# Kernel tuning notes

Measured on AMD Instinct MI355X. Metric: run time of the kernel, lower is better.

Reference implementation:

```python
import jax, jax.numpy as jnp
import numpy as np

DMODEL = 1024
NHEADS = 16
FFN = 4 * DMODEL
HEAD_DIM = DMODEL // NHEADS
SCALE = HEAD_DIM ** -0.5


def layer_norm(x, gamma, beta, eps=1e-5):
    mu = jnp.mean(x, axis=-1, keepdims=True)
    var = jnp.var(x, axis=-1, keepdims=True)
    return (x - mu) * jax.lax.rsqrt(var + eps) * gamma + beta


def setup_inputs() -> dict:
    key = jax.random.key(0)
    ks = jax.random.split(key, 8)
    std = 0.02
    B, S = 2, 2048
    return {
        "src": jax.random.normal(ks[0], (B, S, DMODEL), jnp.float32),
        "pre_gamma": jnp.ones((DMODEL,), jnp.float32),
        "pre_beta": jnp.zeros((DMODEL,), jnp.float32),
        "qkv_w": jax.random.truncated_normal(ks[1], -2.0, 2.0, (3 * DMODEL, DMODEL), jnp.float32) * std,
        "qkv_b": jnp.zeros((3 * DMODEL,), jnp.float32),
        "addnorm_gamma": jnp.ones((DMODEL,), jnp.float32),
        "addnorm_beta": jnp.zeros((DMODEL,), jnp.float32),
        "fc1_w": jax.random.truncated_normal(ks[2], -2.0, 2.0, (FFN, DMODEL), jnp.float32) * std,
        "fc1_b": jnp.zeros((FFN,), jnp.float32),
        "fc2_w": jax.random.truncated_normal(ks[3], -2.0, 2.0, (DMODEL, FFN), jnp.float32) * std,
        "fc2_b": jnp.zeros((DMODEL,), jnp.float32),
    }


def reference(src, pre_gamma, pre_beta, qkv_w, qkv_b, addnorm_gamma, addnorm_beta,
              fc1_w, fc1_b, fc2_w, fc2_b):
    B, S, D = src.shape
    # PreNorm
    x = layer_norm(src, pre_gamma, pre_beta)
    # MHSA (no output projection, matching source)
    qkv = x @ qkv_w.T + qkv_b  # [B,S,3D]
    q, k, v = jnp.split(qkv, 3, axis=-1)
    def heads(t):
        return t.reshape(B, S, NHEADS, HEAD_DIM).transpose(0, 2, 1, 3)  # [B,H,S,hd]
    q, k, v = heads(q), heads(k), heads(v)
    attn = jnp.einsum("bhqd,bhkd->bhqk", q, k) * SCALE
    attn = jax.nn.softmax(attn, axis=-1)
    attn_out = jnp.einsum("bhqk,bhkd->bhqd", attn, v)
    attn_out = attn_out.transpose(0, 2, 1, 3).reshape(B, S, D)
    # shared AddNorm #1
    x = layer_norm(attn_out + x, addnorm_gamma, addnorm_beta)
    # FFN
    h = jax.nn.gelu(x @ fc1_w.T + fc1_b, approximate=False)
    ffn_out = h @ fc2_w.T + fc2_b
    # shared AddNorm #2 (same params as #1)
    return layer_norm(ffn_out + x, addnorm_gamma, addnorm_beta)
```

## Files before the change

### kernel.cpp

```cpp
#include <hip/hip_runtime.h>
#include <hip/hip_bf16.h>
#include <math.h>

#define DMODEL 1024
#define NH 16
#define HD 64
#define SEQ 2048
#define BATCH 2
#define MROWS (BATCH * SEQ)
#define FFN_DIM 4096

using bf16x8 = __attribute__((ext_vector_type(8))) __bf16;
using f32x4  = __attribute__((ext_vector_type(4))) float;

typedef const __attribute__((address_space(1))) unsigned char* gas_t;
typedef __attribute__((address_space(3))) unsigned char* las_t;

__device__ inline unsigned short f2bf(float f) {
    unsigned int u = __builtin_bit_cast(unsigned int, f);
    u += 0x7fffu + ((u >> 16) & 1u);
    return (unsigned short)(u >> 16);
}
__device__ inline unsigned short f2bf_up(float f) {
    unsigned int u = __builtin_bit_cast(unsigned int, f);
    return (unsigned short)((u + 0x8000u) >> 16);
}
__device__ inline float bf2f(unsigned short u) {
    unsigned int v = ((unsigned int)u) << 16;
    return __builtin_bit_cast(float, v);
}
__device__ inline float gelu_f(float x) {
    float x2 = x * x;
    float w = x * fmaf(0.07135481627f, x2, 1.59576912161f);
    return x / (1.0f + __expf(-w));
}

__global__ __launch_bounds__(256) void ln_pre_cvt(
        const float* __restrict__ a,
        const float* __restrict__ gamma, const float* __restrict__ beta,
        float* __restrict__ out_f, unsigned short* __restrict__ out_b,
        const float* __restrict__ wa, unsigned short* __restrict__ oa, int na4,
        const float* __restrict__ wb, unsigned short* __restrict__ ob, int nb4,
        const float* __restrict__ wc, unsigned char* __restrict__ oc, int nc4) {
    int blk = blockIdx.x;
    int t = threadIdx.x;
    if (blk >= MROWS) {
        int i = (blk - MROWS) * 256 + t;
        if (i < na4) {
            float4 v = ((const float4*)wa)[i];
            ushort4 o;
            o.x = f2bf(v.x); o.y = f2bf(v.y); o.z = f2bf(v.z); o.w = f2bf(v.w);
            ((ushort4*)oa)[i] = o;
        } else if (i < na4 + nb4) {
            int j = i - na4;
            float4 v = ((const float4*)wb)[j];
            ushort4 o;
            o.x = f2bf(v.x); o.y = f2bf(v.y); o.z = f2bf(v.z); o.w = f2bf(v.w);
            ((ushort4*)ob)[j] = o;
        } else if (i < na4 + nb4 + nc4) {
            int j = i - na4 - nb4;
            float4 v = ((const float4*)wc)[j];
            int pk = __builtin_amdgcn_cvt_pk_fp8_f32(v.x, v.y, 0, false);
            pk     = __builtin_amdgcn_cvt_pk_fp8_f32(v.z, v.w, pk, true);
            ((unsigned int*)oc)[j] = (unsigned int)pk;
        }
        return;
    }
    int row = blk;
    float4 v = ((const float4*)(a + (size_t)row * DMODEL))[t];
    float s  = v.x + v.y + v.z + v.w;
    float s2 = v.x * v.x + v.y * v.y + v.z * v.z + v.w * v.w;
    #pragma unroll
    for (int off = 32; off > 0; off >>= 1) {
        s  += __shfl_xor(s,  off, 64);
        s2 += __shfl_xor(s2, off, 64);
    }
    __shared__ float red[8];
    int wave = t >> 6, lane = t & 63;
    if (lane == 0) { red[wave] = s; red[4 + wave] = s2; }
    __syncthreads();
    float tot  = red[0] + red[1] + red[2] + red[3];
    float tot2 = red[4] + red[5] + red[6] + red[7];
    float mu   = tot * (1.0f / DMODEL);
    float var  = tot2 * (1.0f / DMODEL) - mu * mu;
    float rstd = rsqrtf(var + 1e-5f);
    float4 g  = ((const float4*)gamma)[t];
    float4 be = ((const float4*)beta)[t];
    float4 o;
    o.x = (v.x - mu) * rstd * g.x + be.x;
    o.y = (v.y - mu) * rstd * g.y + be.y;
    o.z = (v.z - mu) * rstd * g.z + be.z;
    o.w = (v.w - mu) * rstd * g.w + be.w;
    ((float4*)(out_f + (size_t)row * DMODEL))[t] = o;
    ushort4 ob4;
    ob4.x = f2bf(o.x); ob4.y = f2bf(o.y); ob4.z = f2bf(o.z); ob4.w = f2bf(o.w);
    ((ushort4*)(out_b + (size_t)row * DMODEL))[t] = ob4;
}

__global__ __launch_bounds__(256) void ln_attn(
        const float* __restrict__ o0, const float* __restrict__ o1,
        const float* __restrict__ l0, const float* __restrict__ l1,
        const float* __restrict__ xres,
        const float* __restrict__ gamma, const float* __restrict__ beta,
        float* __restrict__ out_f, unsigned short* __restrict__ out_b) {
    int row = blockIdx.x;
    int t = threadIdx.x;
    int b_ = row >> 11, s = row & 2047;
    int h = t >> 4;
    int bh = b_ * NH + h;
    size_t obase = ((size_t)bh * SEQ + s) * HD + (4 * t & 63);
    float4 va = ((const float4*)(o0 + obase))[0];
    float4 vb = ((const float4*)(o1 + obase))[0];
    float inv_l = 1.0f / (l0[(size_t)bh * SEQ + s] + l1[(size_t)bh * SEQ + s]);
    float4 rr = ((const float4*)(xres + (size_t)row * DMODEL))[t];
    float4 v;
    v.x = (va.x + vb.x) * inv_l + rr.x;
    v.y = (va.y + vb.y) * inv_l + rr.y;
    v.z = (va.z + vb.z) * inv_l + rr.z;
    v.w = (va.w + vb.w) * inv_l + rr.w;

    float s1 = v.x + v.y + v.z + v.w;
    float s2 = v.x * v.x + v.y * v.y + v.z * v.z + v.w * v.w;
    #pragma unroll
    for (int off = 32; off > 0; off >>= 1) {
        s1 += __shfl_xor(s1, off, 64);
        s2 += __shfl_xor(s2, off, 64);
    }
    __shared__ float red[8];
    int wave = t >> 6, lane = t & 63;
    if (lane == 0) { red[wave] = s1; red[4 + wave] = s2; }
    __syncthreads();
    float tot  = red[0] + red[1] + red[2] + red[3];
    float tot2 = red[4] + red[5] + red[6] + red[7];
    float mu   = tot * (1.0f / DMODEL);
    float var  = tot2 * (1.0f / DMODEL) - mu * mu;
    float rstd = rsqrtf(var + 1e-5f);
    float4 g  = ((const float4*)gamma)[t];
    float4 be = ((const float4*)beta)[t];
    float4 o;
    o.x = (v.x - mu) * rstd * g.x + be.x;
    o.y = (v.y - mu) * rstd * g.y + be.y;
    o.z = (v.z - mu) * rstd * g.z + be.z;
    o.w = (v.w - mu) * rstd * g.w + be.w;
    ((float4*)(out_f + (size_t)row * DMODEL))[t] = o;
    ushort4 ob;
    ob.x = f2bf(o.x); ob.y = f2bf(o.y); ob.z = f2bf(o.z); ob.w = f2bf(o.w);
    ((ushort4*)(out_b + (size_t)row * DMODEL))[t] = ob;
}

__global__ __launch_bounds__(256) void ln_fc2(
        const unsigned short* __restrict__ p0, const unsigned short* __restrict__ p1,
        const unsigned short* __restrict__ p2, const unsigned short* __restrict__ p3,
        const float* __restrict__ bias, const float* __restrict__ resid,
        const float* __restrict__ gamma, const float* __restrict__ beta,
        float* __restrict__ out_f) {
    int row = blockIdx.x;
    int t = threadIdx.x;
    size_t base = (size_t)row * DMODEL;
    ushort4 u0 = ((const ushort4*)(p0 + base))[t];
    ushort4 u1 = ((const ushort4*)(p1 + base))[t];
    ushort4 u2 = ((const ushort4*)(p2 + base))[t];
    ushort4 u3 = ((const ushort4*)(p3 + base))[t];
    float4 bb = ((const float4*)bias)[t];
    float4 rr = ((const float4*)(resid + base))[t];
    float4 v;
    v.x = bf2f(u0.x) + bf2f(u1.x) + bf2f(u2.x) + bf2f(u3.x) + bb.x + rr.x;
    v.y = bf2f(u0.y) + bf2f(u1.y) + bf2f(u2.y) + bf2f(u3.y) + bb.y + rr.y;
    v.z = bf2f(u0.z) + bf2f(u1.z) + bf2f(u2.z) + bf2f(u3.z) + bb.z + rr.z;
    v.w = bf2f(u0.w) + bf2f(u1.w) + bf2f(u2.w) + bf2f(u3.w) + bb.w + rr.w;

    float s  = v.x + v.y + v.z + v.w;
    float s2 = v.x * v.x + v.y * v.y + v.z * v.z + v.w * v.w;
    #pragma unroll
    for (int off = 32; off > 0; off >>= 1) {
        s  += __shfl_xor(s,  off, 64);
        s2 += __shfl_xor(s2, off, 64);
    }
    __shared__ float red[8];
    int wave = t >> 6, lane = t & 63;
    if (lane == 0) { red[wave] = s; red[4 + wave] = s2; }
    __syncthreads();
    float tot  = red[0] + red[1] + red[2] + red[3];
    float tot2 = red[4] + red[5] + red[6] + red[7];
    float mu   = tot * (1.0f / DMODEL);
    float var  = tot2 * (1.0f / DMODEL) - mu * mu;
    float rstd = rsqrtf(var + 1e-5f);
    float4 g  = ((const float4*)gamma)[t];
    float4 be = ((const float4*)beta)[t];
    float4 o;
    o.x = (v.x - mu) * rstd * g.x + be.x;
    o.y = (v.y - mu) * rstd * g.y + be.y;
    o.z = (v.z - mu) * rstd * g.z + be.z;
    o.w = (v.w - mu) * rstd * g.w + be.w;
    ((float4*)(out_f + base))[t] = o;
}

template <int MODE>
__global__ __launch_bounds__(256) void gemm_lds(
        const unsigned short* __restrict__ A,
        const unsigned short* __restrict__ Bw,
        const float* __restrict__ bias,
        void* __restrict__ out, int M, int N, int K) {
    __shared__ unsigned short As[2][128 * 64];
    __shared__ unsigned short Bs[2][128 * 64];

    const int tid  = threadIdx.x;
    const int wave = tid >> 6;
    const int lane = tid & 63;
    const int quad = lane >> 4;
    const int cc   = lane & 15;
    const int bn = blockIdx.x * 128;
    const int bm = blockIdx.y * 128;

    const unsigned short* Ab = A  + (size_t)bm * K;
    const unsigned short* Bb = Bw + (size_t)bn * K;

    const int srow0 = tid >> 3;
    const int sslot = tid & 7;
    const int rsw   = (cc >> 1) & 7;
    const int wm = (wave >> 1) * 64;
    const int wn = (wave & 1) * 64;

    f32x4 acc[4][4] = {};

    auto stage = [&](int buf, int k0) {
        #pragma unroll
        for (int i = 0; i < 4; ++i) {
            int row = i * 32 + srow0;
            int g   = sslot ^ ((row >> 1) & 7);
            const unsigned short* ga = Ab + (size_t)row * K + k0 + g * 8;
            const unsigned short* gb = Bb + (size_t)row * K + k0 + g * 8;
            unsigned short* la = &As[buf][i * 2048 + wave * 512];
            unsigned short* lb = &Bs[buf][i * 2048 + wave * 512];
            __builtin_amdgcn_global_load_lds((gas_t)(const void*)ga, (las_t)(void*)la, 16, 0, 0);
            __builtin_amdgcn_global_load_lds((gas_t)(const void*)gb, (las_t)(void*)lb, 16, 0, 0);
        }
    };

    const int nkt = K >> 6;
    stage(0, 0);
    __syncthreads();

    int cur = 0;
    for (int kt = 0; kt < nkt; ++kt) {
        if (kt + 1 < nkt) stage(cur ^ 1, (kt + 1) << 6);

        bf16x8 af[4][2], bf[4][2];
        #pragma unroll
        for (int mt = 0; mt < 4; ++mt)
            #pragma unroll
            for (int s = 0; s < 2; ++s) {
                int slot = (s * 4 + quad) ^ rsw;
                af[mt][s] = *(const bf16x8*)&As[cur][(wm + mt * 16 + cc) * 64 + slot * 8];
            }
        #pragma unroll
        for (int nt = 0; nt < 4; ++nt)
            #pragma unroll
            for (int s = 0; s < 2; ++s) {
                int slot = (s * 4 + quad) ^ rsw;
                bf[nt][s] = *(const bf16x8*)&Bs[cur][(wn + nt * 16 + cc) * 64 + slot * 8];
            }

        #pragma unroll
        for (int mt = 0; mt < 4; ++mt)
            #pragma unroll
            for (int nt = 0; nt < 4; ++nt) {
                acc[mt][nt] = __builtin_amdgcn_mfma_f32_16x16x32_bf16(
                    af[mt][0], bf[nt][0], acc[mt][nt], 0, 0, 0);
                acc[mt][nt] = __builtin_amdgcn_mfma_f32_16x16x32_bf16(
                    af[mt][1], bf[nt][1], acc[mt][nt], 0, 0, 0);
            }

        if (kt + 1 < nkt) __syncthreads();
        cur ^= 1;
    }

    #pragma unroll
    for (int mt = 0; mt < 4; ++mt)
        #pragma unroll
        for (int nt = 0; nt < 4; ++nt) {
            if constexpr (MODE == 1) {
                int m0 = bm + wm + mt * 16 + quad * 4;
                int n  = bn + wn + nt * 16 + cc;
                float bn_ = bias[n];
                float v0 = gelu_f(acc[mt][nt][0] + bn_);
                float v1 = gelu_f(acc[mt][nt][1] + bn_);
                float v2 = gelu_f(acc[mt][nt][2] + bn_);
                float v3 = gelu_f(acc[mt][nt][3] + bn_);
                int pk = __builtin_amdgcn_cvt_pk_fp8_f32(v0, v1, 0, false);
                pk     = __builtin_amdgcn_cvt_pk_fp8_f32(v2, v3, pk, true);
                unsigned char* o = (unsigned char*)out + (size_t)m0 * N + n;
                o[0]             = (unsigned char)pk;
                o[(size_t)N]     = (unsigned char)(pk >> 8);
                o[(size_t)2 * N] = (unsigned char)(pk >> 16);
                o[(size_t)3 * N] = (unsigned char)(pk >> 24);
            } else {
                #pragma unroll
                for (int r = 0; r < 4; ++r) {
                    int m = bm + wm + mt * 16 + quad * 4 + r;
                    int n = bn + wn + nt * 16 + cc;
                    float v = acc[mt][nt][r] + bias[n];
                    int b_ = m >> 11, srow = m & 2047;
                    int which = n >> 10, rem = n & 1023;
                    int h = rem >> 6, d = rem & 63;
                    if (which == 0) v *= 0.125f;
                    size_t idx = ((((size_t)which * BATCH + b_) * NH + h) * SEQ + srow) * HD + d;
                    ((unsigned short*)out)[idx] = f2bf(v);
                }
            }
        }
}

__global__ __launch_bounds__(256) void gemm_fp8(
        const unsigned char* __restrict__ A,
        const unsigned char* __restrict__ Bw,
        unsigned short* __restrict__ p0, unsigned short* __restrict__ p1,
        unsigned short* __restrict__ p2, unsigned short* __restrict__ p3,
        int M, int N, int K, int KC) {
    __shared__ unsigned char As[3][128 * 64];
    __shared__ unsigned char Bs[3][128 * 64];

    const int tid  = threadIdx.x;
    const int wave = tid >> 6;
    const int lane = tid & 63;
    const int quad = lane >> 4;
    const int cc   = lane & 15;
    const int bn = blockIdx.x * 128;
    const int bm = blockIdx.y * 128;

    const unsigned char* Ab = A  + (size_t)bm * K;
    const unsigned char* Bb = Bw + (size_t)bn * K;

    const int srow0 = tid >> 2;
    const int schunk = tid & 3;
    const int rsw = (cc >> 1) & 3;
    const int wm = (wave >> 1) * 64;
    const int wn = (wave & 1) * 64;

    const int kbeg = blockIdx.z * KC;

    f32x4 acc[4][4] = {};

    auto stage = [&](int buf, int k0) {
        #pragma unroll
        for (int i = 0; i < 2; ++i) {
            int row = i * 64 + srow0;
            int g   = schunk ^ ((row >> 1) & 3);
            const unsigned char* ga = Ab + (size_t)row * K + k0 + g * 16;
            const unsigned char* gb = Bb + (size_t)row * K + k0 + g * 16;
            unsigned char* la = &As[buf][i * 4096 + wave * 1024];
            unsigned char* lb = &Bs[buf][i * 4096 + wave * 1024];
            __builtin_amdgcn_global_load_lds((gas_t)(const void*)ga, (las_t)(void*)la, 16, 0, 0);
            __builtin_amdgcn_global_load_lds((gas_t)(const void*)gb, (las_t)(void*)lb, 16, 0, 0);
        }
    };

    const int nkt = KC >> 6;
    stage(0, kbeg);
    if (nkt > 1) {
        stage(1, kbeg + 64);
        asm volatile("s_waitcnt vmcnt(4)" ::: "memory");
    } else {
        asm volatile("s_waitcnt vmcnt(0)" ::: "memory");
    }
    __builtin_amdgcn_s_barrier();

    int cur = 0;
    for (int kt = 0; kt < nkt; ++kt) {
        int pbuf = cur + 2; if (pbuf >= 3) pbuf -= 3;
        if (kt + 2 < nkt) stage(pbuf, kbeg + ((kt + 2) << 6));

        long af[4][2], bf[4][2];
        #pragma unroll
        for (int mt = 0; mt < 4; ++mt)
            #pragma unroll
            for (int s = 0; s < 2; ++s) {
                int slot = ((quad >> 1) + 2 * s) ^ rsw;
                af[mt][s] = *(const long*)&As[cur][(wm + mt * 16 + cc) * 64 + slot * 16 + (quad & 1) * 8];
            }
        #pragma unroll
        for (int nt = 0; nt < 4; ++nt)
            #pragma unroll
            for (int s = 0; s < 2; ++s) {
                int slot = ((quad >> 1) + 2 * s) ^ rsw;
                bf[nt][s] = *(const long*)&Bs[cur][(wn + nt * 16 + cc) * 64 + slot * 16 + (quad & 1) * 8];
            }

        #pragma unroll
        for (int mt = 0; mt < 4; ++mt)
            #pragma unroll
            for (int nt = 0; nt < 4; ++nt) {
                acc[mt][nt] = __builtin_amdgcn_mfma_f32_16x16x32_fp8_fp8(
                    af[mt][0], bf[nt][0], acc[mt][nt], 0, 0, 0);
                acc[mt][nt] = __builtin_amdgcn_mfma_f32_16x16x32_fp8_fp8(
                    af[mt][1], bf[nt][1], acc[mt][nt], 0, 0, 0);
            }

        if (kt + 1 < nkt) {
            asm volatile("s_waitcnt lgkmcnt(0)" ::: "memory");
            if (kt + 2 < nkt)
                asm volatile("s_waitcnt vmcnt(4)" ::: "memory");
            else
                asm volatile("s_waitcnt vmcnt(0)" ::: "memory");
            __builtin_amdgcn_s_barrier();
        }
        cur = (cur < 2) ? cur + 1 : 0;
    }

    unsigned short* outp = (blockIdx.z == 0) ? p0
                         : (blockIdx.z == 1) ? p1
                         : (blockIdx.z == 2) ? p2 : p3;
    #pragma unroll
    for (int mt = 0; mt < 4; ++mt)
        #pragma unroll
        for (int nt = 0; nt < 4; ++nt)
            #pragma unroll
            for (int r = 0; r < 4; ++r) {
                int m = bm + wm + mt * 16 + quad * 4 + r;
                int n = bn + wn + nt * 16 + cc;
                outp[(size_t)m * N + n] = f2bf(acc[mt][nt][r]);
            }
}

__global__ __launch_bounds__(256) void transpose_v(
        const unsigned short* __restrict__ vsrc, unsigned short* __restrict__ vt) {
    __shared__ unsigned short Ls[64 * 72];
    const int t = threadIdx.x;
    const int s0 = blockIdx.x * 64;
    const int bh = blockIdx.y;
    const unsigned short* in = vsrc + (size_t)bh * SEQ * HD;
    unsigned short* outp = vt + (size_t)bh * SEQ * HD;

    const int row = t >> 2;
    const int c8  = (t & 3) * 8;
    #pragma unroll
    for (int p = 0; p < 2; ++p)
        *(uint4*)&Ls[row * 72 + c8 + p * 32] =
            *(const uint4*)&in[(size_t)(s0 + row) * HD + c8 + p * 32];
    __syncthreads();

    const int hd = t >> 2;
    #pragma unroll
    for (int p = 0; p < 2; ++p) {
        unsigned short tmp[8];
        #pragma unroll
        for (int j = 0; j < 8; ++j)
            tmp[j] = Ls[(c8 + p * 32 + j) * 72 + hd];
        *(uint4*)&outp[(size_t)hd * SEQ + s0 + c8 + p * 32] = *(uint4*)tmp;
    }
}

#define KPAD 72
__global__ __launch_bounds__(256, 4) void attn_mfma(
        const unsigned short* __restrict__ qkv,
        const unsigned short* __restrict__ vt,
        float* __restrict__ op0, float* __restrict__ op1,
        float* __restrict__ lpart) {
    const int tid  = threadIdx.x;
    const int wave = tid >> 6;
    const int lane = tid & 63;
    const int quad = lane >> 4;
    const int cc   = lane & 15;
    const int qblk = blockIdx.x;
    const int bh   = blockIdx.y;
    const int half = blockIdx.z;

    const size_t headsz = (size_t)SEQ * HD;
    const unsigned short* qb  = qkv + (size_t)bh * headsz;
    const unsigned short* kb  = qkv + ((size_t)BATCH * NH + bh) * headsz;
    const unsigned short* vtb = vt + (size_t)bh * headsz;
    float* opart = half ? op1 : op0;
    float* lp    = lpart + (size_t)half * BATCH * NH * SEQ;

    __shared__ unsigned short Ks[64 * 64];
    __shared__ unsigned short Vt[64 * 64];
    __shared__ unsigned short Ps[4 * 32 * KPAD];

    bf16x8 qa[2][2];
    #pragma unroll
    for (int mt = 0; mt < 2; ++mt) {
        const unsigned short* qp =
            qb + (size_t)(qblk * 128 + wave * 32 + mt * 16 + cc) * HD + quad * 8;
        qa[mt][0] = *(const bf16x8*)qp;
        qa[mt][1] = *(const bf16x8*)(qp + 32);
    }

    f32x4 o_acc[2][4] = {};
    float l_i[2][4] = {};

    const int srow0 = wave * 16 + (lane >> 3);
    const int sc8c  = lane & 7;
    const int swz   = (sc8c ^ (lane >> 3)) * 8;
    const int psw   = (cc >> 2) & 3;
    const int rw7   = cc & 7;

    const int kt0 = half * 16, ktend = kt0 + 16;

    uint4 ka0, ka1, va0, va1;
    {
        const unsigned short* kp0 = &kb[(size_t)(kt0 * 64 + srow0) * HD + sc8c * 8];
        const unsigned short* vp0 = &vtb[(size_t)srow0 * SEQ + kt0 * 64 + sc8c * 8];
        ka0 = *(const uint4*)kp0;
        ka1 = *(const uint4*)(kp0 + 8 * HD);
        va0 = *(const uint4*)vp0;
        va1 = *(const uint4*)(vp0 + 8 * SEQ);
    }

    for (int kt = kt0; kt < ktend; ++kt) {
        __syncthreads();
        *(uint4*)&Ks[srow0 * 64 + swz]        = ka0;
        *(uint4*)&Ks[(srow0 + 8) * 64 + swz]  = ka1;
        *(uint4*)&Vt[srow0 * 64 + swz]        = va0;
        *(uint4*)&Vt[(srow0 + 8) * 64 + swz]  = va1;
        __syncthreads();

        int ktn = (kt + 1 < ktend) ? kt + 1 : kt;
        const unsigned short* kpn = &kb[(size_t)(ktn * 64 + srow0) * HD + sc8c * 8];
        const unsigned short* vpn = &vtb[(size_t)srow0 * SEQ + ktn * 64 + sc8c * 8];
        uint4 nk0 = *(const uint4*)kpn;
        uint4 nk1 = *(const uint4*)(kpn + 8 * HD);
        uint4 nv0 = *(const uint4*)vpn;
        uint4 nv1 = *(const uint4*)(vpn + 8 * SEQ);

        f32x4 s_acc[2][4];
        #pragma unroll
        for (int nt = 0; nt < 4; ++nt) {
            const unsigned short* kp = &Ks[(nt * 16 + cc) * 64];
            bf16x8 kf0 = *(const bf16x8*)&kp[(quad ^ rw7) * 8];
            bf16x8 kf1 = *(const bf16x8*)&kp[((quad + 4) ^ rw7) * 8];
            #pragma unroll
            for (int mt = 0; mt < 2; ++mt) {
                f32x4 z = {};
                z = __builtin_amdgcn_mfma_f32_16x16x32_bf16(qa[mt][0], kf0, z, 0, 0, 0);
                s_acc[mt][nt] = __builtin_amdgcn_mfma_f32_16x16x32_bf16(qa[mt][1], kf1, z, 0, 0, 0);
            }
        }

        unsigned short* pw = &Ps[wave * 32 * KPAD];
        #pragma unroll
        for (int mt = 0; mt < 2; ++mt)
            #pragma unroll
            for (int nt = 0; nt < 4; ++nt) {
                int pc = ((nt ^ quad) & 3) * 16 + cc;
                #pragma unroll
                for (int r = 0; r < 4; ++r) {
                    float e = __expf(s_acc[mt][nt][r]);
                    l_i[mt][r] += e;
                    pw[(mt * 16 + quad * 4 + r) * KPAD + pc] = f2bf_up(e);
                }
            }

        bf16x8 pf[2][2];
        #pragma unroll
        for (int mt = 0; mt < 2; ++mt) {
            const unsigned short* pa = &pw[(mt * 16 + cc) * KPAD];
            pf[mt][0] = *(const bf16x8*)&pa[((((quad >> 1))     ^ psw) & 3) * 16 + (quad & 1) * 8];
            pf[mt][1] = *(const bf16x8*)&pa[(((2 + (quad >> 1)) ^ psw) & 3) * 16 + (quad & 1) * 8];
        }

        #pragma unroll
        for (int nt = 0; nt < 4; ++nt) {
            const unsigned short* vp = &Vt[(nt * 16 + cc) * 64];
            bf16x8 vf0 = *(const bf16x8*)&vp[(quad ^ rw7) * 8];
            bf16x8 vf1 = *(const bf16x8*)&vp[((quad + 4) ^ rw7) * 8];
            #pragma unroll
            for (int mt = 0; mt < 2; ++mt) {
                o_acc[mt][nt] = __builtin_amdgcn_mfma_f32_16x16x32_bf16(
                    pf[mt][0], vf0, o_acc[mt][nt], 0, 0, 0);
                o_acc[mt][nt] = __builtin_amdgcn_mfma_f32_16x16x32_bf16(
                    pf[mt][1], vf1, o_acc[mt][nt], 0, 0, 0);
            }
        }

        ka0 = nk0; ka1 = nk1; va0 = nv0; va1 = nv1;
    }

    #pragma unroll
    for (int mt = 0; mt < 2; ++mt) {
        float lr[4];
        #pragma unroll
        for (int r = 0; r < 4; ++r) {
            float l = l_i[mt][r];
            #pragma unroll
            for (int off = 1; off < 16; off <<= 1)
                l += __shfl_xor(l, off, 64);
            lr[r] = l;
        }
        int rowbase = qblk * 128 + wave * 32 + mt * 16;
        if (cc == 0) {
            float4 lv = {lr[0], lr[1], lr[2], lr[3]};
            *(float4*)&lp[(size_t)bh * SEQ + rowbase + quad * 4] = lv;
        }
        #pragma unroll
        for (int nt = 0; nt < 4; ++nt)
            #pragma unroll
            for (int r = 0; r < 4; ++r) {
                int row = rowbase + quad * 4 + r;
                opart[((size_t)bh * SEQ + row) * HD + nt * 16 + cc] = o_acc[mt][nt][r];
            }
    }
}

extern "C" void kernel_launch(void* const* d_in, const int* in_sizes, int n_in,
                              void* d_out, int out_size, void* d_ws, size_t ws_size,
                              hipStream_t stream) {
    const float* src       = (const float*)d_in[0];
    const float* pre_gamma = (const float*)d_in[1];
    const float* pre_beta  = (const float*)d_in[2];
    const float* qkv_w     = (const float*)d_in[3];
    const float* qkv_b     = (const float*)d_in[4];
    const float* an_gamma  = (const float*)d_in[5];
    const float* an_beta   = (const float*)d_in[6];
    const float* fc1_w     = (const float*)d_in[7];
    const float* fc1_b     = (const float*)d_in[8];
    const float* fc2_w     = (const float*)d_in[9];
    const float* fc2_b     = (const float*)d_in[10];
    float* out = (float*)d_out;

    char* ws = (char*)d_ws;
    size_t off = 0;
    auto alloc = [&](size_t bytes) {
        char* p = ws + off;
        off += (bytes + 255) & ~(size_t)255;
        return p;
    };
    float*          x_f   = (float*)alloc((size_t)MROWS * DMODEL * 4);
    unsigned short* x_b   = (unsigned short*)alloc((size_t)MROWS * DMODEL * 2);
    float*          y_f   = (float*)alloc((size_t)MROWS * DMODEL * 4);
    unsigned short* y_b   = (unsigned short*)alloc((size_t)MROWS * DMODEL * 2);
    float*          atf   = (float*)alloc((size_t)MROWS * DMODEL * 4);
    float*          fff   = (float*)alloc((size_t)MROWS * DMODEL * 4);
    unsigned short* qkvb  = (unsigned short*)alloc((size_t)3 * MROWS * DMODEL * 2);
    unsigned char*  h8    = (unsigned char*)alloc((size_t)MROWS * FFN_DIM * 2);
    unsigned short* wqkv  = (unsigned short*)alloc((size_t)3 * DMODEL * DMODEL * 2);
    unsigned short* wfc1  = (unsigned short*)alloc((size_t)FFN_DIM * DMODEL * 2);
    unsigned char*  wfc28 = (unsigned char*)alloc((size_t)DMODEL * FFN_DIM);

    unsigned short* vt_b = (unsigned short*)fff;
    float* opart0 = atf;
    float* opart1 = (float*)h8;
    float* lpart  = (float*)x_b;
    unsigned short* fc2p0 = (unsigned short*)fff;
    unsigned short* fc2p1 = (unsigned short*)x_f;
    unsigned short* fc2p2 = (unsigned short*)atf;
    unsigned short* fc2p3 = (unsigned short*)qkvb;

    int n_qkv4 = 3 * DMODEL * DMODEL / 4;
    int n_fc4  = FFN_DIM * DMODEL / 4;
    int cvt_blocks = (n_qkv4 + 2 * n_fc4 + 255) / 256;

    ln_pre_cvt<<<dim3(MROWS + cvt_blocks), dim3(256), 0, stream>>>(
        src, pre_gamma, pre_beta, x_f, x_b,
        qkv_w, wqkv, n_qkv4, fc1_w, wfc1, n_fc4, fc2_w, wfc28, n_fc4);

    gemm_lds<3><<<dim3(3 * DMODEL / 128, MROWS / 128), dim3(256), 0, stream>>>(
        x_b, wqkv, qkv_b, qkvb, MROWS, 3 * DMODEL, DMODEL);
    transpose_v<<<dim3(SEQ / 64, BATCH * NH), dim3(256), 0, stream>>>(
        qkvb + (size_t)2 * BATCH * NH * SEQ * HD, vt_b);
    attn_mfma<<<dim3(SEQ / 128, BATCH * NH, 2), dim3(256), 0, stream>>>(
        qkvb, vt_b, opart0, opart1, lpart);
    ln_attn<<<dim3(MROWS), dim3(256), 0, stream>>>(
        opart0, opart1, lpart, lpart + (size_t)BATCH * NH * SEQ,
        x_f, an_gamma, an_beta, y_f, y_b);
    gemm_lds<1><<<dim3(FFN_DIM / 128, MROWS / 128), dim3(256), 0, stream>>>(
        y_b, wfc1, fc1_b, h8, MROWS, FFN_DIM, DMODEL);
    gemm_fp8<<<dim3(DMODEL / 128, MROWS / 128, 4), dim3(256), 0, stream>>>(
        h8, wfc28, fc2p0, fc2p1, fc2p2, fc2p3, MROWS, DMODEL, FFN_DIM, 1024);
    ln_fc2<<<dim3(MROWS), dim3(256), 0, stream>>>(
        fc2p0, fc2p1, fc2p2, fc2p3, fc2_b, y_f, an_gamma, an_beta, out);
}
```

Baseline: 318.1 us.

## Switch GEMM to triple-buffered BK=32 pipeline with explicit vmcnt waits

Changes the LDS-staged GEMM from double-buffered 64-wide K tiles to triple-buffered 32-wide K tiles, prefetching two stages ahead. Replaces __syncthreads with explicit s_waitcnt vmcnt/lgkmcnt plus s_barrier so only the oldest outstanding loads are waited on. The aim is to hide more global-load latency behind MFMA work. In exchange it halves the compute per iteration, doubles the barrier count, and relies on hand-counted vmcnt values that must match the number of issued loads.

```diff
diff --git a/kernel.cpp b/kernel.cpp
--- a/kernel.cpp
+++ b/kernel.cpp
@@ -201,8 +201,8 @@
         const unsigned short* __restrict__ Bw,
         const float* __restrict__ bias,
         void* __restrict__ out, int M, int N, int K) {
-    __shared__ unsigned short As[2][128 * 64];
-    __shared__ unsigned short Bs[2][128 * 64];
+    __shared__ unsigned short As[3][128 * 32];
+    __shared__ unsigned short Bs[3][128 * 32];
 
     const int tid  = threadIdx.x;
     const int wave = tid >> 6;
@@ -215,9 +215,9 @@
     const unsigned short* Ab = A  + (size_t)bm * K;
     const unsigned short* Bb = Bw + (size_t)bn * K;
 
-    const int srow0 = tid >> 3;
-    const int sslot = tid & 7;
-    const int rsw   = (cc >> 1) & 7;
+    const int srow0  = tid >> 2;
+    const int schunk = tid & 3;
+    const int rsw    = (cc >> 1) & 3;
     const int wm = (wave >> 1) * 64;
     const int wn = (wave & 1) * 64;
 
@@ -225,9 +225,9 @@
 
     auto stage = [&](int buf, int k0) {
         #pragma unroll
-        for (int i = 0; i < 4; ++i) {
-            int row = i * 32 + srow0;
-            int g   = sslot ^ ((row >> 1) & 7);
+        for (int i = 0; i < 2; ++i) {
+            int row = i * 64 + srow0;
+            int g   = schunk ^ ((row >> 1) & 3);
             const unsigned short* ga = Ab + (size_t)row * K + k0 + g * 8;
             const unsigned short* gb = Bb + (size_t)row * K + k0 + g * 8;
             unsigned short* la = &As[buf][i * 2048 + wave * 512];
@@ -237,42 +237,45 @@
         }
     };
 
-    const int nkt = K >> 6;
+    const int nkt = K >> 5;
     stage(0, 0);
-    __syncthreads();
+    if (nkt > 1) {
+        stage(1, 32);
+        asm volatile("s_waitcnt vmcnt(4)" ::: "memory");
+    } else {
+        asm volatile("s_waitcnt vmcnt(0)" ::: "memory");
+    }
+    __builtin_amdgcn_s_barrier();
 
     int cur = 0;
     for (int kt = 0; kt < nkt; ++kt) {
-        if (kt + 1 < nkt) stage(cur ^ 1, (kt + 1) << 6);
-
-        bf16x8 af[4][2], bf[4][2];
+        int pbuf = cur + 2; if (pbuf >= 3) pbuf -= 3;
+        if (kt + 2 < nkt) stage(pbuf, (kt + 2) << 5);
+
+        bf16x8 af[4], bf[4];
         #pragma unroll
         for (int mt = 0; mt < 4; ++mt)
-            #pragma unroll
-            for (int s = 0; s < 2; ++s) {
-                int slot = (s * 4 + quad) ^ rsw;
-                af[mt][s] = *(const bf16x8*)&As[cur][(wm + mt * 16 + cc) * 64 + slot * 8];
-            }
+            af[mt] = *(const bf16x8*)&As[cur][(wm + mt * 16 + cc) * 32 + ((quad ^ rsw) * 8)];
         #pragma unroll
         for (int nt = 0; nt < 4; ++nt)
-            #pragma unroll
-            for (int s = 0; s < 2; ++s) {
-                int slot = (s * 4 + quad) ^ rsw;
-                bf[nt][s] = *(const bf16x8*)&Bs[cur][(wn + nt * 16 + cc) * 64 + slot * 8];
-            }
+            bf[nt] = *(const bf16x8*)&Bs[cur][(wn + nt * 16 + cc) * 32 + ((quad ^ rsw) * 8)];
 
         #pragma unroll
         for (int mt = 0; mt < 4; ++mt)
             #pragma unroll
-            for (int nt = 0; nt < 4; ++nt) {
+            for (int nt = 0; nt < 4; ++nt)
                 acc[mt][nt] = __builtin_amdgcn_mfma_f32_16x16x32_bf16(
-                    af[mt][0], bf[nt][0], acc[mt][nt], 0, 0, 0);
-                acc[mt][nt] = __builtin_amdgcn_mfma_f32_16x16x32_bf16(
-                    af[mt][1], bf[nt][1], acc[mt][nt], 0, 0, 0);
-            }
-
-        if (kt + 1 < nkt) __syncthreads();
-        cur ^= 1;
+                    af[mt], bf[nt], acc[mt][nt], 0, 0, 0);
+
+        if (kt + 1 < nkt) {
+            asm volatile("s_waitcnt lgkmcnt(0)" ::: "memory");
+            if (kt + 2 < nkt)
+                asm volatile("s_waitcnt vmcnt(4)" ::: "memory");
+            else
+                asm volatile("s_waitcnt vmcnt(0)" ::: "memory");
+            __builtin_amdgcn_s_barrier();
+        }
+        cur = (cur < 2) ? cur + 1 : 0;
     }
 
     #pragma unroll
```

After: 326.7 us. +2.7%, slower.
